# Kernel optimization log

Hardware: AMD Instinct MI355X
Metric: run time of the kernel (lower is better)

## Reference

```python
import jax, jax.numpy as jnp
import numpy as np

DIM = 512
HIDDEN = int(DIM * 0.2)  # 102
K_TOKENS = 64
N_TOKENS = 65536
LN_EPS = 1e-5


def setup_inputs() -> dict:
    key = jax.random.key(0)
    ks = jax.random.split(key, 8)
    x = jax.random.normal(ks[0], (N_TOKENS, DIM), dtype=jnp.float32)
    ln_gamma = jnp.ones((DIM,), dtype=jnp.float32)
    ln_beta = jnp.zeros((DIM,), dtype=jnp.float32)
    W1 = jax.random.normal(ks[1], (DIM, HIDDEN), dtype=jnp.float32) / np.sqrt(DIM)
    b1 = jnp.zeros((HIDDEN,), dtype=jnp.float32)
    W2 = jax.random.normal(ks[2], (HIDDEN, K_TOKENS), dtype=jnp.float32) / np.sqrt(HIDDEN)
    b2 = jnp.zeros((K_TOKENS,), dtype=jnp.float32)
    scale = jnp.ones((1, 1), dtype=jnp.float32)
    return {
        "x": x,
        "ln_gamma": ln_gamma,
        "ln_beta": ln_beta,
        "W1": W1,
        "b1": b1,
        "W2": W2,
        "b2": b2,
        "scale": scale,
        "keeped_tokens": K_TOKENS,
    }


def reference(x, ln_gamma, ln_beta, W1, b1, W2, b2, scale, keeped_tokens):
    # LayerNorm over last dim
    mu = jnp.mean(x, axis=-1, keepdims=True)
    var = jnp.mean(jnp.square(x - mu), axis=-1, keepdims=True)
    h = (x - mu) * jax.lax.rsqrt(var + LN_EPS) * ln_gamma + ln_beta
    # fc1 + exact GELU (torch default) + dynamic fc2 scorer
    h = jax.nn.gelu(h @ W1 + b1, approximate=False)  # [N, HIDDEN]
    w = h @ W2 + b2                                   # [N, K]
    # transpose, scale, softmax over tokens
    w = w.T * scale                                   # [K, N]
    w = jax.nn.softmax(w, axis=1)
    # weighted token aggregation
    return w @ x                                      # [K, DIM]
```

## Files before the change

### kernel.cpp

```cpp
#include <hip/hip_runtime.h>
#include <math.h>

#define N_TOK 65536
#define DIM   512
#define HID   102
#define KTOK  64
#define NTILE 4096
#define LN_EPS 1e-5f

typedef __attribute__((ext_vector_type(8))) short short8;
typedef __attribute__((ext_vector_type(4))) float f32x4;

#define WS_LOGITS 0u
#define WS_PART   4194304u
#define WS_PM     (WS_PART + 4194304u)
#define WS_PS     (WS_PM + 262144u)
#define WS_W1F    (WS_PS + 262144u)
#define WS_W2F    (WS_W1F + 32768u)
#define WS_UB     (WS_W2F + 4096u)
#define WS_VV     (WS_UB + 128u)
#define WS_SMAX   (WS_VV + 128u)
#define WS_SINV   (WS_SMAX + 64u)

__device__ __forceinline__ unsigned short f2bf(float f) {
    unsigned int u = __float_as_uint(f);
    unsigned int r = (u + 0x7fffu + ((u >> 16) & 1u)) >> 16;
    return (unsigned short)r;
}
__device__ __forceinline__ float bf2f(unsigned short h) {
    return __uint_as_float(((unsigned int)h) << 16);
}

__device__ __forceinline__ void gload_lds16(const void* g, void* l) {
    __builtin_amdgcn_global_load_lds(
        (const __attribute__((address_space(1))) unsigned int*)g,
        (__attribute__((address_space(3))) unsigned int*)l, 16, 0, 0);
}

__device__ __forceinline__ void bar_lds() {
    asm volatile("s_waitcnt lgkmcnt(0)" ::: "memory");
    __builtin_amdgcn_s_barrier();
    __builtin_amdgcn_sched_barrier(0);
}

__global__ __launch_bounds__(256) void prep_k(const float* __restrict__ W1,
                                              const float* __restrict__ gamma,
                                              const float* __restrict__ W2,
                                              unsigned short* __restrict__ W1f,
                                              unsigned short* __restrict__ W2f) {
    const int idx = blockIdx.x * 256 + threadIdx.x;
    {
        const int e = idx & 7, lane = (idx >> 3) & 63;
        const int jj = (idx >> 9) & 7, kc = (idx >> 12) & 15;
        const int j = jj * 16 + (lane & 15);
        const int d = kc * 32 + (lane >> 4) * 8 + e;
        W1f[idx] = (j < HID) ? f2bf(gamma[d] * W1[d * HID + j]) : (unsigned short)0;
    }
    if (idx < 8192) {
        const int e = idx & 7, lane = (idx >> 3) & 63;
        const int kc = (idx >> 9) & 3, N = (idx >> 11) & 3;
        const int j = kc * 32 + (lane >> 4) * 8 + e;
        const int k = N * 16 + (lane & 15);
        W2f[idx] = (j < HID) ? f2bf(W2[j * KTOK + k]) : (unsigned short)0;
    }
}

__global__ __launch_bounds__(512) void prep2_k(const float* __restrict__ W1,
                                               const float* __restrict__ b1,
                                               const float* __restrict__ gamma,
                                               const float* __restrict__ beta,
                                               float* __restrict__ ub,
                                               float* __restrict__ vv) {
    __shared__ float su[4][128], sv[4][128];
    const int t = threadIdx.x;
    const int j = t & 127, q = t >> 7;
    float u = 0.0f, v = 0.0f;
    if (j < HID) {
        #pragma unroll 8
        for (int d = q * 128; d < q * 128 + 128; ++d) {
            const float wv = W1[d * HID + j];
            u = fmaf(beta[d], wv, u);
            v = fmaf(gamma[d], wv, v);
        }
    }
    su[q][j] = u; sv[q][j] = v;
    __syncthreads();
    if (q == 0) {
        ub[j] = su[0][j] + su[1][j] + su[2][j] + su[3][j] +
                ((j < HID) ? b1[j] : 0.0f);
        vv[j] = sv[0][j] + sv[1][j] + sv[2][j] + sv[3][j];
    }
}

__global__ __launch_bounds__(256) void scorer_k(const float* __restrict__ x,
                                                const unsigned short* __restrict__ W1f,
                                                const unsigned short* __restrict__ W2f,
                                                const float* __restrict__ ub,
                                                const float* __restrict__ vv,
                                                const float* __restrict__ b2,
                                                const float* __restrict__ scale,
                                                float* __restrict__ logits,
                                                float* __restrict__ pm,
                                                float* __restrict__ psum) {
    __shared__ char smem[3 * 8192];
    const int tid = threadIdx.x;
    const int lane = tid & 63;
    const int w = tid >> 6;
    const int l15 = lane & 15;
    const int hi = lane >> 4;
    const int tile = blockIdx.x * 4 + w;
    const int wt0 = tile * 16;
    char* hb = smem + w * 4096;

    const float* xrow = x + (size_t)(wt0 + l15) * DIM + hi * 8;

    f32x4 xva[3], xvb[3];
    xva[0] = *(const f32x4*)(xrow);
    xvb[0] = *(const f32x4*)(xrow + 4);
    xva[1] = *(const f32x4*)(xrow + 32);
    xvb[1] = *(const f32x4*)(xrow + 36);
    gload_lds16(W1f + w * 1024 + lane * 8, smem + w * 2048);
    gload_lds16(W1f + w * 1024 + 512 + lane * 8, smem + w * 2048 + 1024);
    gload_lds16(W1f + 4096 + w * 1024 + lane * 8, smem + 8192 + w * 2048);
    gload_lds16(W1f + 4096 + w * 1024 + 512 + lane * 8, smem + 8192 + w * 2048 + 1024);

    f32x4 acc[8] = {};
    float s = 0.0f, ss = 0.0f;
    #pragma unroll
    for (int kc = 0; kc < 16; ++kc) {
        if (kc < 14) {
            xva[(kc + 2) % 3] = *(const f32x4*)(xrow + (kc + 2) * 32);
            xvb[(kc + 2) % 3] = *(const f32x4*)(xrow + (kc + 2) * 32 + 4);
            const unsigned short* sn = W1f + (kc + 2) * 4096 + w * 1024 + lane * 8;
            gload_lds16(sn, smem + ((kc + 2) % 3) * 8192 + w * 2048);
            gload_lds16(sn + 512, smem + ((kc + 2) % 3) * 8192 + w * 2048 + 1024);
        }
        if (kc == 0)       asm volatile("s_waitcnt vmcnt(6)" ::: "memory");
        else if (kc <= 13) asm volatile("s_waitcnt vmcnt(8)" ::: "memory");
        else if (kc == 14) asm volatile("s_waitcnt vmcnt(4)" ::: "memory");
        else               asm volatile("s_waitcnt vmcnt(0)" ::: "memory");
        __builtin_amdgcn_sched_barrier(0);
        __builtin_amdgcn_s_barrier();
        const f32x4 a = xva[kc % 3];
        const f32x4 b = xvb[kc % 3];
        s += a.x + a.y + a.z + a.w + b.x + b.y + b.z + b.w;
        ss += a.x * a.x + a.y * a.y + a.z * a.z + a.w * a.w +
              b.x * b.x + b.y * b.y + b.z * b.z + b.w * b.w;
        short8 af;
        af[0] = (short)f2bf(a.x); af[1] = (short)f2bf(a.y);
        af[2] = (short)f2bf(a.z); af[3] = (short)f2bf(a.w);
        af[4] = (short)f2bf(b.x); af[5] = (short)f2bf(b.y);
        af[6] = (short)f2bf(b.z); af[7] = (short)f2bf(b.w);
        const char* bb = smem + (kc % 3) * 8192 + lane * 16;
        __builtin_amdgcn_s_setprio(1);
        #pragma unroll
        for (int jj = 0; jj < 8; ++jj) {
            const short8 bf = *(const short8*)(bb + jj * 1024);
            acc[jj] = __builtin_amdgcn_mfma_f32_16x16x32_bf16(af, bf, acc[jj], 0, 0, 0);
        }
        __builtin_amdgcn_s_setprio(0);
    }
    __syncthreads();

    s += __shfl_xor(s, 16); ss += __shfl_xor(ss, 16);
    s += __shfl_xor(s, 32); ss += __shfl_xor(ss, 32);
    const float mu = s * (1.0f / 512.0f);
    const float inv = rsqrtf(ss * (1.0f / 512.0f) - mu * mu + LN_EPS);

    float invr[4], muir[4];
    #pragma unroll
    for (int r = 0; r < 4; ++r) {
        const int tk = 4 * hi + r;
        const float m_ = __shfl(mu, tk);
        const float i_ = __shfl(inv, tk);
        invr[r] = i_;
        muir[r] = m_ * i_;
    }
    #pragma unroll
    for (int jj = 0; jj < 8; ++jj) {
        const int col = jj * 16 + l15;
        const float ubj = ub[col];
        const float vvj = vv[col];
        #pragma unroll
        for (int reg = 0; reg < 4; ++reg) {
            const int t = 4 * hi + reg;
            const float pre = fmaf(invr[reg], acc[jj][reg],
                                   fmaf(-muir[reg], vvj, ubj));
            const float g = 0.5f * pre * (1.0f + erff(pre * 0.70710678118f));
            *(unsigned short*)(hb + t * 256 + ((col * 2) ^ ((t & 7) << 4))) = f2bf(g);
        }
    }
    asm volatile("s_waitcnt lgkmcnt(0)" ::: "memory");
    __builtin_amdgcn_sched_barrier(0);

    f32x4 acc2[4] = {};
    {
        const unsigned short* w2 = W2f + lane * 8;
        #pragma unroll
        for (int kc = 0; kc < 4; ++kc) {
            const short8 a2 = *(const short8*)(hb + l15 * 256 +
                                               ((kc * 64 + hi * 16) ^ ((l15 & 7) << 4)));
            __builtin_amdgcn_s_setprio(1);
            #pragma unroll
            for (int nt = 0; nt < 4; ++nt) {
                const short8 bfr = *(const short8*)(w2 + (size_t)(nt * 4 + kc) * 512);
                acc2[nt] = __builtin_amdgcn_mfma_f32_16x16x32_bf16(a2, bfr, acc2[nt], 0, 0, 0);
            }
            __builtin_amdgcn_s_setprio(0);
        }
    }

    const float sc = scale[0];
    #pragma unroll
    for (int nt = 0; nt < 4; ++nt) {
        const int k = nt * 16 + l15;
        const float bb = b2[k];
        f32x4 lv;
        lv.x = (acc2[nt][0] + bb) * sc;
        lv.y = (acc2[nt][1] + bb) * sc;
        lv.z = (acc2[nt][2] + bb) * sc;
        lv.w = (acc2[nt][3] + bb) * sc;
        *(f32x4*)(logits + (size_t)k * N_TOK + wt0 + hi * 4) = lv;
        float m4 = fmaxf(fmaxf(lv.x, lv.y), fmaxf(lv.z, lv.w));
        float s4 = __expf(lv.x - m4) + __expf(lv.y - m4) +
                   __expf(lv.z - m4) + __expf(lv.w - m4);
        #pragma unroll
        for (int o = 16; o <= 32; o <<= 1) {
            const float om = __shfl_xor(m4, o);
            const float os = __shfl_xor(s4, o);
            const float nm = fmaxf(m4, om);
            s4 = s4 * __expf(m4 - nm) + os * __expf(om - nm);
            m4 = nm;
        }
        if (hi == 0) {
            pm[tile * 64 + k] = m4;
            psum[tile * 64 + k] = s4;
        }
    }
}

__global__ __launch_bounds__(256) void stats_k(const float* __restrict__ pm,
                                               const float* __restrict__ psum,
                                               float* __restrict__ smax,
                                               float* __restrict__ sinv) {
    const int k = blockIdx.x;
    const int tid = threadIdx.x;
    __shared__ float rm[4], rs[4];
    float m = -1e30f, s = 0.0f;
    for (int b = tid; b < NTILE; b += 256) {
        const float pmv = pm[b * 64 + k];
        const float psv = psum[b * 64 + k];
        const float nm = fmaxf(m, pmv);
        s = s * __expf(m - nm) + psv * __expf(pmv - nm);
        m = nm;
    }
    #pragma unroll
    for (int o = 32; o >= 1; o >>= 1) {
        const float om = __shfl_xor(m, o);
        const float os = __shfl_xor(s, o);
        const float nm = fmaxf(m, om);
        s = s * __expf(m - nm) + os * __expf(om - nm);
        m = nm;
    }
    if ((tid & 63) == 0) { rm[tid >> 6] = m; rs[tid >> 6] = s; }
    __syncthreads();
    if (tid == 0) {
        float fm = rm[0], fs = rs[0];
        for (int i = 1; i < 4; ++i) {
            const float nm = fmaxf(fm, rm[i]);
            fs = fs * __expf(fm - nm) + rs[i] * __expf(rm[i] - nm);
            fm = nm;
        }
        smax[k] = fm;
        sinv[k] = 1.0f / fs;
    }
}

__global__ __launch_bounds__(512) void agg_k(const float* __restrict__ x,
                                             const float* __restrict__ logits,
                                             const float* __restrict__ smax,
                                             const float* __restrict__ sinv,
                                             float* __restrict__ part) {
    __shared__ char fsm[40960];
    const int tid = threadIdx.x;
    const int lane = tid & 63;
    const int w = tid >> 6;
    const int l15 = lane & 15;
    const int hi = lane >> 4;
    const int dg = blockIdx.y;
    const int tb = blockIdx.x;

    const int sk = tid >> 3;
    const int snp = (tid & 7) * 8;
    const int xd = tid & 127;
    const int xnb = (tid >> 7) * 16;
    const float mk = smax[sk];
    const float ik = sinv[sk];
    const float* lrow = logits + (size_t)sk * N_TOK + tb * 512 + snp;
    const float* xcol = x + (size_t)(tb * 512 + xnb) * DIM + dg * 128 + xd;

    char* pw = fsm + (((sk >> 4) * 2 + (snp >> 5)) * 64 +
                      (sk & 15) + 16 * ((snp & 31) >> 3)) * 16;
    const int xoff0 = (((xd >> 4) * 2 + (xnb >> 5)) * 64 +
                       (xd & 15) + 16 * (((xnb & 31) >> 3) + 0)) * 16;
    const int xoff1 = (((xd >> 4) * 2 + (xnb >> 5)) * 64 +
                       (xd & 15) + 16 * (((xnb & 31) >> 3) + 1)) * 16;

    const int kt = w & 3;
    const int dgr = w >> 2;

    f32x4 acc[4] = {};

    f32x4 pa = *(const f32x4*)(lrow);
    f32x4 pb = *(const f32x4*)(lrow + 4);
    float xl[16];
    #pragma unroll
    for (int i = 0; i < 16; ++i) xl[i] = xcol[(size_t)i * DIM];

    for (int c = 0; c < 8; ++c) {
        {
            short8 pv;
            pv[0] = (short)f2bf(__expf(pa.x - mk) * ik);
            pv[1] = (short)f2bf(__expf(pa.y - mk) * ik);
            pv[2] = (short)f2bf(__expf(pa.z - mk) * ik);
            pv[3] = (short)f2bf(__expf(pa.w - mk) * ik);
            pv[4] = (short)f2bf(__expf(pb.x - mk) * ik);
            pv[5] = (short)f2bf(__expf(pb.y - mk) * ik);
            pv[6] = (short)f2bf(__expf(pb.z - mk) * ik);
            pv[7] = (short)f2bf(__expf(pb.w - mk) * ik);
            *(short8*)pw = pv;
        }
        {
            short8 h0, l0, h1, l1;
            #pragma unroll
            for (int e = 0; e < 8; ++e) {
                const float v = xl[e];
                const unsigned short hb16 = f2bf(v);
                h0[e] = (short)hb16;
                l0[e] = (short)f2bf(v - bf2f(hb16));
            }
            #pragma unroll
            for (int e = 0; e < 8; ++e) {
                const float v = xl[8 + e];
                const unsigned short hb16 = f2bf(v);
                h1[e] = (short)hb16;
                l1[e] = (short)f2bf(v - bf2f(hb16));
            }
            *(short8*)(fsm + 8192 + xoff0) = h0;
            *(short8*)(fsm + 24576 + xoff0) = l0;
            *(short8*)(fsm + 8192 + xoff1) = h1;
            *(short8*)(fsm + 24576 + xoff1) = l1;
        }
        f32x4 pa_n, pb_n;
        float xln[16];
        if (c < 7) {
            pa_n = *(const f32x4*)(lrow + (c + 1) * 64);
            pb_n = *(const f32x4*)(lrow + (c + 1) * 64 + 4);
            #pragma unroll
            for (int i = 0; i < 16; ++i)
                xln[i] = xcol[(size_t)((c + 1) * 64 + i) * DIM];
        }
        bar_lds();

        __builtin_amdgcn_s_setprio(1);
        #pragma unroll
        for (int ns = 0; ns < 2; ++ns) {
            const short8 af =
                *(const short8*)(fsm + ((kt * 2 + ns) * 64 + lane) * 16);
            #pragma unroll
            for (int dt = 0; dt < 4; ++dt) {
                const int dti = dgr * 4 + dt;
                const short8 bh = *(const short8*)(fsm + 8192 +
                                                   ((dti * 2 + ns) * 64 + lane) * 16);
                const short8 bl = *(const short8*)(fsm + 24576 +
                                                   ((dti * 2 + ns) * 64 + lane) * 16);
                acc[dt] = __builtin_amdgcn_mfma_f32_16x16x32_bf16(af, bh, acc[dt], 0, 0, 0);
                acc[dt] = __builtin_amdgcn_mfma_f32_16x16x32_bf16(af, bl, acc[dt], 0, 0, 0);
            }
        }
        __builtin_amdgcn_s_setprio(0);
        bar_lds();

        pa = pa_n; pb = pb_n;
        #pragma unroll
        for (int i = 0; i < 16; ++i) xl[i] = xln[i];
    }

    #pragma unroll
    for (int dt = 0; dt < 4; ++dt) {
        const int dcol = dg * 128 + (dgr * 4 + dt) * 16 + l15;
        #pragma unroll
        for (int reg = 0; reg < 4; ++reg) {
            const int k = kt * 16 + 4 * hi + reg;
            part[((size_t)tb * 64 + k) * 512 + dcol] = acc[dt][reg];
        }
    }
}

__global__ __launch_bounds__(256) void reduce_k(const float* __restrict__ part,
                                                float* __restrict__ out) {
    const int idx = blockIdx.x * 256 + threadIdx.x;
    const int k = idx >> 9, d = idx & 511;
    float s = 0.0f;
    for (int tb = 0; tb < 128; ++tb) s += part[((size_t)tb * 64 + k) * 512 + d];
    out[idx] = s;
}

extern "C" void kernel_launch(void* const* d_in, const int* in_sizes, int n_in,
                              void* d_out, int out_size, void* d_ws, size_t ws_size,
                              hipStream_t stream) {
    const float* x     = (const float*)d_in[0];
    const float* gamma = (const float*)d_in[1];
    const float* beta  = (const float*)d_in[2];
    const float* W1    = (const float*)d_in[3];
    const float* b1    = (const float*)d_in[4];
    const float* W2    = (const float*)d_in[5];
    const float* b2    = (const float*)d_in[6];
    const float* scale = (const float*)d_in[7];
    float* out = (float*)d_out;
    float* ws  = (float*)d_ws;

    float* logits = ws + WS_LOGITS;
    float* part   = ws + WS_PART;
    float* pm     = ws + WS_PM;
    float* psum   = ws + WS_PS;
    unsigned short* W1f = (unsigned short*)(ws + WS_W1F);
    unsigned short* W2f = (unsigned short*)(ws + WS_W2F);
    float* ubv  = ws + WS_UB;
    float* vvv  = ws + WS_VV;
    float* smax = ws + WS_SMAX;
    float* sinv = ws + WS_SINV;

    hipLaunchKernelGGL(prep_k, dim3(256), dim3(256), 0, stream,
                       W1, gamma, W2, W1f, W2f);
    hipLaunchKernelGGL(prep2_k, dim3(1), dim3(512), 0, stream,
                       W1, b1, gamma, beta, ubv, vvv);
    hipLaunchKernelGGL(scorer_k, dim3(NTILE / 4), dim3(256), 0, stream,
                       x, W1f, W2f, ubv, vvv, b2, scale, logits, pm, psum);
    hipLaunchKernelGGL(stats_k, dim3(KTOK), dim3(256), 0, stream,
                       pm, psum, smax, sinv);
    hipLaunchKernelGGL(agg_k, dim3(128, 4), dim3(512), 0, stream,
                       x, logits, smax, sinv, part);
    hipLaunchKernelGGL(reduce_k, dim3(128), dim3(256), 0, stream,
                       part, out);
}
```

Baseline: 104.9 us.

## Load W1 fragments directly into registers instead of staging through LDS

```diff
diff --git a/kernel.cpp b/kernel.cpp
--- a/kernel.cpp
+++ b/kernel.cpp
@@ -102,7 +102,7 @@
                                                 float* __restrict__ logits,
                                                 float* __restrict__ pm,
                                                 float* __restrict__ psum) {
-    __shared__ char smem[3 * 8192];
+    __shared__ char hsm[4][4096];
     const int tid = threadIdx.x;
     const int lane = tid & 63;
     const int w = tid >> 6;
@@ -110,57 +110,65 @@
     const int hi = lane >> 4;
     const int tile = blockIdx.x * 4 + w;
     const int wt0 = tile * 16;
-    char* hb = smem + w * 4096;
+    char* hb = &hsm[w][0];
 
     const float* xrow = x + (size_t)(wt0 + l15) * DIM + hi * 8;
-
-    f32x4 xva[3], xvb[3];
+    const unsigned short* wb = W1f + lane * 8;
+
+    f32x4 xva[2], xvb[2];
+    short8 bf[3][4];
     xva[0] = *(const f32x4*)(xrow);
     xvb[0] = *(const f32x4*)(xrow + 4);
-    xva[1] = *(const f32x4*)(xrow + 32);
-    xvb[1] = *(const f32x4*)(xrow + 36);
-    gload_lds16(W1f + w * 1024 + lane * 8, smem + w * 2048);
-    gload_lds16(W1f + w * 1024 + 512 + lane * 8, smem + w * 2048 + 1024);
-    gload_lds16(W1f + 4096 + w * 1024 + lane * 8, smem + 8192 + w * 2048);
-    gload_lds16(W1f + 4096 + w * 1024 + 512 + lane * 8, smem + 8192 + w * 2048 + 1024);
+    __builtin_amdgcn_sched_barrier(0);
+    #pragma unroll
+    for (int j = 0; j < 4; ++j) bf[0][j] = *(const short8*)(wb + j * 512);
+    __builtin_amdgcn_sched_barrier(0);
+    #pragma unroll
+    for (int j = 0; j < 4; ++j) bf[1][j] = *(const short8*)(wb + (4 + j) * 512);
+    __builtin_amdgcn_sched_barrier(0);
 
     f32x4 acc[8] = {};
     float s = 0.0f, ss = 0.0f;
-    #pragma unroll
-    for (int kc = 0; kc < 16; ++kc) {
-        if (kc < 14) {
-            xva[(kc + 2) % 3] = *(const f32x4*)(xrow + (kc + 2) * 32);
-            xvb[(kc + 2) % 3] = *(const f32x4*)(xrow + (kc + 2) * 32 + 4);
-            const unsigned short* sn = W1f + (kc + 2) * 4096 + w * 1024 + lane * 8;
-            gload_lds16(sn, smem + ((kc + 2) % 3) * 8192 + w * 2048);
-            gload_lds16(sn + 512, smem + ((kc + 2) % 3) * 8192 + w * 2048 + 1024);
-        }
-        if (kc == 0)       asm volatile("s_waitcnt vmcnt(6)" ::: "memory");
-        else if (kc <= 13) asm volatile("s_waitcnt vmcnt(8)" ::: "memory");
-        else if (kc == 14) asm volatile("s_waitcnt vmcnt(4)" ::: "memory");
-        else               asm volatile("s_waitcnt vmcnt(0)" ::: "memory");
+    short8 af;
+    #pragma unroll
+    for (int h = 0; h < 32; ++h) {
+        const int kc = h >> 1;
+        if ((h & 1) == 0 && kc + 1 < 16) {
+            xva[(kc + 1) & 1] = *(const f32x4*)(xrow + (kc + 1) * 32);
+            xvb[(kc + 1) & 1] = *(const f32x4*)(xrow + (kc + 1) * 32 + 4);
+            __builtin_amdgcn_sched_barrier(0);
+        }
+        if (h + 2 < 32) {
+            const int kcn = (h + 2) >> 1, half = (h + 2) & 1;
+            #pragma unroll
+            for (int j = 0; j < 4; ++j)
+                bf[(h + 2) % 3][j] =
+                    *(const short8*)(wb + kcn * 4096 + (half * 4 + j) * 512);
+            __builtin_amdgcn_sched_barrier(0);
+        }
+        if (h <= 29)      asm volatile("s_waitcnt vmcnt(10)" ::: "memory");
+        else if (h == 30) asm volatile("s_waitcnt vmcnt(4)" ::: "memory");
+        else              asm volatile("s_waitcnt vmcnt(0)" ::: "memory");
         __builtin_amdgcn_sched_barrier(0);
-        __builtin_amdgcn_s_barrier();
-        const f32x4 a = xva[kc % 3];
-        const f32x4 b = xvb[kc % 3];
-        s += a.x + a.y + a.z + a.w + b.x + b.y + b.z + b.w;
-        ss += a.x * a.x + a.y * a.y + a.z * a.z + a.w * a.w +
-              b.x * b.x + b.y * b.y + b.z * b.z + b.w * b.w;
-        short8 af;
-        af[0] = (short)f2bf(a.x); af[1] = (short)f2bf(a.y);
-        af[2] = (short)f2bf(a.z); af[3] = (short)f2bf(a.w);
-        af[4] = (short)f2bf(b.x); af[5] = (short)f2bf(b.y);
-        af[6] = (short)f2bf(b.z); af[7] = (short)f2bf(b.w);
-        const char* bb = smem + (kc % 3) * 8192 + lane * 16;
+        if ((h & 1) == 0) {
+            const f32x4 a = xva[kc & 1];
+            const f32x4 b = xvb[kc & 1];
+            s += a.x + a.y + a.z + a.w + b.x + b.y + b.z + b.w;
+            ss += a.x * a.x + a.y * a.y + a.z * a.z + a.w * a.w +
+                  b.x * b.x + b.y * b.y + b.z * b.z + b.w * b.w;
+            af[0] = (short)f2bf(a.x); af[1] = (short)f2bf(a.y);
+            af[2] = (short)f2bf(a.z); af[3] = (short)f2bf(a.w);
+            af[4] = (short)f2bf(b.x); af[5] = (short)f2bf(b.y);
+            af[6] = (short)f2bf(b.z); af[7] = (short)f2bf(b.w);
+        }
         __builtin_amdgcn_s_setprio(1);
         #pragma unroll
-        for (int jj = 0; jj < 8; ++jj) {
-            const short8 bf = *(const short8*)(bb + jj * 1024);
-            acc[jj] = __builtin_amdgcn_mfma_f32_16x16x32_bf16(af, bf, acc[jj], 0, 0, 0);
+        for (int j = 0; j < 4; ++j) {
+            const int jj = (h & 1) * 4 + j;
+            acc[jj] = __builtin_amdgcn_mfma_f32_16x16x32_bf16(af, bf[h % 3][j], acc[jj], 0, 0, 0);
         }
         __builtin_amdgcn_s_setprio(0);
     }
-    __syncthreads();
 
     s += __shfl_xor(s, 16); ss += __shfl_xor(ss, 16);
     s += __shfl_xor(s, 32); ss += __shfl_xor(ss, 32);
```

Result: no change. 106.1 us (+1.1%).

## Process two 16-token tiles per wave in scorer to reuse W1 LDS loads

Applied to the files above, without the earlier changes.

```diff
diff --git a/kernel.cpp b/kernel.cpp
--- a/kernel.cpp
+++ b/kernel.cpp
@@ -102,109 +102,85 @@
                                                 float* __restrict__ logits,
                                                 float* __restrict__ pm,
                                                 float* __restrict__ psum) {
-    __shared__ char smem[3 * 8192];
+    __shared__ char smem[3 * 8192 + 4 * 4096];
     const int tid = threadIdx.x;
     const int lane = tid & 63;
     const int w = tid >> 6;
     const int l15 = lane & 15;
     const int hi = lane >> 4;
-    const int tile = blockIdx.x * 4 + w;
-    const int wt0 = tile * 16;
-    char* hb = smem + w * 4096;
-
-    const float* xrow = x + (size_t)(wt0 + l15) * DIM + hi * 8;
-
-    f32x4 xva[3], xvb[3];
-    xva[0] = *(const f32x4*)(xrow);
-    xvb[0] = *(const f32x4*)(xrow + 4);
-    xva[1] = *(const f32x4*)(xrow + 32);
-    xvb[1] = *(const f32x4*)(xrow + 36);
+    const int tile0 = blockIdx.x * 8 + w * 2;
+    char* hb = smem + 24576 + w * 4096;
+
+    const float* xr0 = x + (size_t)(tile0 * 16 + l15) * DIM + hi * 8;
+    const float* xr1 = xr0 + 16 * DIM;
+
+    f32x4 a0[3], b0[3], a1[3], b1v[3];
+    a0[0] = *(const f32x4*)(xr0);
+    b0[0] = *(const f32x4*)(xr0 + 4);
+    a1[0] = *(const f32x4*)(xr1);
+    b1v[0] = *(const f32x4*)(xr1 + 4);
+    a0[1] = *(const f32x4*)(xr0 + 32);
+    b0[1] = *(const f32x4*)(xr0 + 36);
+    a1[1] = *(const f32x4*)(xr1 + 32);
+    b1v[1] = *(const f32x4*)(xr1 + 36);
     gload_lds16(W1f + w * 1024 + lane * 8, smem + w * 2048);
     gload_lds16(W1f + w * 1024 + 512 + lane * 8, smem + w * 2048 + 1024);
     gload_lds16(W1f + 4096 + w * 1024 + lane * 8, smem + 8192 + w * 2048);
     gload_lds16(W1f + 4096 + w * 1024 + 512 + lane * 8, smem + 8192 + w * 2048 + 1024);
 
-    f32x4 acc[8] = {};
-    float s = 0.0f, ss = 0.0f;
+    f32x4 acc0[8] = {}, acc1[8] = {};
+    float s0 = 0.0f, ss0 = 0.0f, s1 = 0.0f, ss1 = 0.0f;
     #pragma unroll
     for (int kc = 0; kc < 16; ++kc) {
         if (kc < 14) {
-            xva[(kc + 2) % 3] = *(const f32x4*)(xrow + (kc + 2) * 32);
-            xvb[(kc + 2) % 3] = *(const f32x4*)(xrow + (kc + 2) * 32 + 4);
+            a0[(kc + 2) % 3] = *(const f32x4*)(xr0 + (kc + 2) * 32);
+            b0[(kc + 2) % 3] = *(const f32x4*)(xr0 + (kc + 2) * 32 + 4);
+            a1[(kc + 2) % 3] = *(const f32x4*)(xr1 + (kc + 2) * 32);
+            b1v[(kc + 2) % 3] = *(const f32x4*)(xr1 + (kc + 2) * 32 + 4);
             const unsigned short* sn = W1f + (kc + 2) * 4096 + w * 1024 + lane * 8;
             gload_lds16(sn, smem + ((kc + 2) % 3) * 8192 + w * 2048);
             gload_lds16(sn + 512, smem + ((kc + 2) % 3) * 8192 + w * 2048 + 1024);
         }
-        if (kc == 0)       asm volatile("s_waitcnt vmcnt(6)" ::: "memory");
-        else if (kc <= 13) asm volatile("s_waitcnt vmcnt(8)" ::: "memory");
-        else if (kc == 14) asm volatile("s_waitcnt vmcnt(4)" ::: "memory");
+        if (kc == 0)       asm volatile("s_waitcnt vmcnt(8)" ::: "memory");
+        else if (kc <= 13) asm volatile("s_waitcnt vmcnt(12)" ::: "memory");
+        else if (kc == 14) asm volatile("s_waitcnt vmcnt(6)" ::: "memory");
         else               asm volatile("s_waitcnt vmcnt(0)" ::: "memory");
         __builtin_amdgcn_sched_barrier(0);
         __builtin_amdgcn_s_barrier();
-        const f32x4 a = xva[kc % 3];
-        const f32x4 b = xvb[kc % 3];
-        s += a.x + a.y + a.z + a.w + b.x + b.y + b.z + b.w;
-        ss += a.x * a.x + a.y * a.y + a.z * a.z + a.w * a.w +
-              b.x * b.x + b.y * b.y + b.z * b.z + b.w * b.w;
-        short8 af;
-        af[0] = (short)f2bf(a.x); af[1] = (short)f2bf(a.y);
-        af[2] = (short)f2bf(a.z); af[3] = (short)f2bf(a.w);
-        af[4] = (short)f2bf(b.x); af[5] = (short)f2bf(b.y);
-        af[6] = (short)f2bf(b.z); af[7] = (short)f2bf(b.w);
         const char* bb = smem + (kc % 3) * 8192 + lane * 16;
-        __builtin_amdgcn_s_setprio(1);
-        #pragma unroll
-        for (int jj = 0; jj < 8; ++jj) {
-            const short8 bf = *(const short8*)(bb + jj * 1024);
-            acc[jj] = __builtin_amdgcn_mfma_f32_16x16x32_bf16(af, bf, acc[jj], 0, 0, 0);
-        }
-        __builtin_amdgcn_s_setprio(0);
-    }
-    __syncthreads();
-
-    s += __shfl_xor(s, 16); ss += __shfl_xor(ss, 16);
-    s += __shfl_xor(s, 32); ss += __shfl_xor(ss, 32);
-    const float mu = s * (1.0f / 512.0f);
-    const float inv = rsqrtf(ss * (1.0f / 512.0f) - mu * mu + LN_EPS);
-
-    float invr[4], muir[4];
-    #pragma unroll
-    for (int r = 0; r < 4; ++r) {
-        const int tk = 4 * hi + r;
-        const float m_ = __shfl(mu, tk);
-        const float i_ = __shfl(inv, tk);
-        invr[r] = i_;
-        muir[r] = m_ * i_;
-    }
-    #pragma unroll
-    for (int jj = 0; jj < 8; ++jj) {
-        const int col = jj * 16 + l15;
-        const float ubj = ub[col];
-        const float vvj = vv[col];
-        #pragma unroll
-        for (int reg = 0; reg < 4; ++reg) {
-            const int t = 4 * hi + reg;
-            const float pre = fmaf(invr[reg], acc[jj][reg],
-                                   fmaf(-muir[reg], vvj, ubj));
-            const float g = 0.5f * pre * (1.0f + erff(pre * 0.70710678118f));
-            *(unsigned short*)(hb + t * 256 + ((col * 2) ^ ((t & 7) << 4))) = f2bf(g);
-        }
-    }
-    asm volatile("s_waitcnt lgkmcnt(0)" ::: "memory");
-    __builtin_amdgcn_sched_barrier(0);
-
-    f32x4 acc2[4] = {};
-    {
-        const unsigned short* w2 = W2f + lane * 8;
-        #pragma unroll
-        for (int kc = 0; kc < 4; ++kc) {
-            const short8 a2 = *(const short8*)(hb + l15 * 256 +
-                                               ((kc * 64 + hi * 16) ^ ((l15 & 7) << 4)));
+        {
+            const f32x4 a = a0[kc % 3], b = b0[kc % 3];
+            s0 += a.x + a.y + a.z + a.w + b.x + b.y + b.z + b.w;
+            ss0 += a.x * a.x + a.y * a.y + a.z * a.z + a.w * a.w +
+                   b.x * b.x + b.y * b.y + b.z * b.z + b.w * b.w;
+            short8 af;
+            af[0] = (short)f2bf(a.x); af[1] = (short)f2bf(a.y);
+            af[2] = (short)f2bf(a.z); af[3] = (short)f2bf(a.w);
+            af[4] = (short)f2bf(b.x); af[5] = (short)f2bf(b.y);
+            af[6] = (short)f2bf(b.z); af[7] = (short)f2bf(b.w);
             __builtin_amdgcn_s_setprio(1);
             #pragma unroll
-            for (int nt = 0; nt < 4; ++nt) {
-                const short8 bfr = *(const short8*)(w2 + (size_t)(nt * 4 + kc) * 512);
-                acc2[nt] = __builtin_amdgcn_mfma_f32_16x16x32_bf16(a2, bfr, acc2[nt], 0, 0, 0);
+            for (int jj = 0; jj < 8; ++jj) {
+                const short8 bf = *(const short8*)(bb + jj * 1024);
+                acc0[jj] = __builtin_amdgcn_mfma_f32_16x16x32_bf16(af, bf, acc0[jj], 0, 0, 0);
+            }
+            __builtin_amdgcn_s_setprio(0);
+        }
+        {
+            const f32x4 a = a1[kc % 3], b = b1v[kc % 3];
+            s1 += a.x + a.y + a.z + a.w + b.x + b.y + b.z + b.w;
+            ss1 += a.x * a.x + a.y * a.y + a.z * a.z + a.w * a.w +
+                   b.x * b.x + b.y * b.y + b.z * b.z + b.w * b.w;
+            short8 af;
+            af[0] = (short)f2bf(a.x); af[1] = (short)f2bf(a.y);
+            af[2] = (short)f2bf(a.z); af[3] = (short)f2bf(a.w);
+            af[4] = (short)f2bf(b.x); af[5] = (short)f2bf(b.y);
+            af[6] = (short)f2bf(b.z); af[7] = (short)f2bf(b.w);
+            __builtin_amdgcn_s_setprio(1);
+            #pragma unroll
+            for (int jj = 0; jj < 8; ++jj) {
+                const short8 bf = *(const short8*)(bb + jj * 1024);
+                acc1[jj] = __builtin_amdgcn_mfma_f32_16x16x32_bf16(af, bf, acc1[jj], 0, 0, 0);
             }
             __builtin_amdgcn_s_setprio(0);
         }
@@ -212,29 +188,84 @@
 
     const float sc = scale[0];
     #pragma unroll
-    for (int nt = 0; nt < 4; ++nt) {
-        const int k = nt * 16 + l15;
-        const float bb = b2[k];
-        f32x4 lv;
-        lv.x = (acc2[nt][0] + bb) * sc;
-        lv.y = (acc2[nt][1] + bb) * sc;
-        lv.z = (acc2[nt][2] + bb) * sc;
-        lv.w = (acc2[nt][3] + bb) * sc;
-        *(f32x4*)(logits + (size_t)k * N_TOK + wt0 + hi * 4) = lv;
-        float m4 = fmaxf(fmaxf(lv.x, lv.y), fmaxf(lv.z, lv.w));
-        float s4 = __expf(lv.x - m4) + __expf(lv.y - m4) +
-                   __expf(lv.z - m4) + __expf(lv.w - m4);
-        #pragma unroll
-        for (int o = 16; o <= 32; o <<= 1) {
-            const float om = __shfl_xor(m4, o);
-            const float os = __shfl_xor(s4, o);
-            const float nm = fmaxf(m4, om);
-            s4 = s4 * __expf(m4 - nm) + os * __expf(om - nm);
-            m4 = nm;
-        }
-        if (hi == 0) {
-            pm[tile * 64 + k] = m4;
-            psum[tile * 64 + k] = s4;
+    for (int t = 0; t < 2; ++t) {
+        const int tile = tile0 + t;
+        const int wt0 = tile * 16;
+        float s = t ? s1 : s0, ss = t ? ss1 : ss0;
+        s += __shfl_xor(s, 16); ss += __shfl_xor(ss, 16);
+        s += __shfl_xor(s, 32); ss += __shfl_xor(ss, 32);
+        const float mu = s * (1.0f / 512.0f);
+        const float inv = rsqrtf(ss * (1.0f / 512.0f) - mu * mu + LN_EPS);
+
+        float invr[4], muir[4];
+        #pragma unroll
+        for (int r = 0; r < 4; ++r) {
+            const int tk = 4 * hi + r;
+            const float m_ = __shfl(mu, tk);
+            const float i_ = __shfl(inv, tk);
+            invr[r] = i_;
+            muir[r] = m_ * i_;
+        }
+        #pragma unroll
+        for (int jj = 0; jj < 8; ++jj) {
+            const int col = jj * 16 + l15;
+            const float ubj = ub[col];
+            const float vvj = vv[col];
+            #pragma unroll
+            for (int reg = 0; reg < 4; ++reg) {
+                const int tk = 4 * hi + reg;
+                const float av = t ? acc1[jj][reg] : acc0[jj][reg];
+                const float pre = fmaf(invr[reg], av, fmaf(-muir[reg], vvj, ubj));
+                const float g = 0.5f * pre * (1.0f + erff(pre * 0.70710678118f));
+                *(unsigned short*)(hb + tk * 256 + ((col * 2) ^ ((tk & 7) << 4))) =
+                    f2bf(g);
+            }
+        }
+        asm volatile("s_waitcnt lgkmcnt(0)" ::: "memory");
+        __builtin_amdgcn_sched_barrier(0);
+
+        f32x4 acc2[4] = {};
+        {
+            const unsigned short* w2 = W2f + lane * 8;
+            #pragma unroll
+            for (int kc = 0; kc < 4; ++kc) {
+                const short8 a2 = *(const short8*)(hb + l15 * 256 +
+                                                   ((kc * 64 + hi * 16) ^ ((l15 & 7) << 4)));
+                __builtin_amdgcn_s_setprio(1);
+                #pragma unroll
+                for (int nt = 0; nt < 4; ++nt) {
+                    const short8 bfr = *(const short8*)(w2 + (size_t)(nt * 4 + kc) * 512);
+                    acc2[nt] = __builtin_amdgcn_mfma_f32_16x16x32_bf16(a2, bfr, acc2[nt], 0, 0, 0);
+                }
+                __builtin_amdgcn_s_setprio(0);
+            }
+        }
+
+        #pragma unroll
+        for (int nt = 0; nt < 4; ++nt) {
+            const int k = nt * 16 + l15;
+            const float bb = b2[k];
+            f32x4 lv;
+            lv.x = (acc2[nt][0] + bb) * sc;
+            lv.y = (acc2[nt][1] + bb) * sc;
+            lv.z = (acc2[nt][2] + bb) * sc;
+            lv.w = (acc2[nt][3] + bb) * sc;
+            *(f32x4*)(logits + (size_t)k * N_TOK + wt0 + hi * 4) = lv;
+            float m4 = fmaxf(fmaxf(lv.x, lv.y), fmaxf(lv.z, lv.w));
+            float s4 = __expf(lv.x - m4) + __expf(lv.y - m4) +
+                       __expf(lv.z - m4) + __expf(lv.w - m4);
+            #pragma unroll
+            for (int o = 16; o <= 32; o <<= 1) {
+                const float om = __shfl_xor(m4, o);
+                const float os = __shfl_xor(s4, o);
+                const float nm = fmaxf(m4, om);
+                s4 = s4 * __expf(m4 - nm) + os * __expf(om - nm);
+                m4 = nm;
+            }
+            if (hi == 0) {
+                pm[tile * 64 + k] = m4;
+                psum[tile * 64 + k] = s4;
+            }
         }
     }
 }
@@ -435,7 +466,7 @@
                        W1, gamma, W2, W1f, W2f);
     hipLaunchKernelGGL(prep2_k, dim3(1), dim3(512), 0, stream,
                        W1, b1, gamma, beta, ubv, vvv);
-    hipLaunchKernelGGL(scorer_k, dim3(NTILE / 4), dim3(256), 0, stream,
+    hipLaunchKernelGGL(scorer_k, dim3(NTILE / 8), dim3(256), 0, stream,
                        x, W1f, W2f, ubv, vvv, b2, scale, logits, pm, psum);
     hipLaunchKernelGGL(stats_k, dim3(KTOK), dim3(256), 0, stream,
                        pm, psum, smax, sinv);
```

Measured after the change: 123.9 us. 18.1% more time.
